# Kernel tuning notes

Measured on AMD Instinct MI355X. Metric: run time of the kernel, lower is better.

Reference implementation:

```python
import jax, jax.numpy as jnp
import numpy as np

B, N, D_IN = 128, 128, 1024
H1, D_OUT = 256, 32
K = 8  # num_clusters


def setup_inputs() -> dict:
    key = jax.random.key(0)
    ks = jax.random.split(key, 3)
    x = jax.random.normal(ks[0], (B, N, D_IN), dtype=jnp.float32)
    W1 = jax.random.normal(ks[1], (D_IN, H1), dtype=jnp.float32) * (1.0 / np.sqrt(D_IN))
    b1 = jnp.zeros((H1,), jnp.float32)
    W2 = jax.random.normal(ks[2], (H1, D_OUT), dtype=jnp.float32) * (1.0 / np.sqrt(H1))
    b2 = jnp.zeros((D_OUT,), jnp.float32)
    return {"x": x, "W1": W1, "b1": b1, "W2": W2, "b2": b2}


def _mlp(x, W1, b1, W2, b2):
    # nn.Sequential(GELU, Linear(1024,256), GELU, Linear(256,32)); torch GELU default = exact erf
    h = jax.nn.gelu(x, approximate=False)
    h = h @ W1 + b1
    h = jax.nn.gelu(h, approximate=False)
    return h @ W2 + b2  # [B, N, 32]


def _ward_labels(feats, k):
    """Greedy ward-linkage agglomerative clustering of feats [n, d] -> int labels [n].
    Ward merge cost d(A,B) = |A||B|/(|A|+|B|) * ||c_A - c_B||^2 (Lance-Williams equiv)."""
    n = feats.shape[0]
    eye = jnp.eye(n, dtype=bool)

    def body(t, state):
        cents, sizes, lab = state
        sq = jnp.sum(cents * cents, axis=-1)
        d2 = jnp.maximum(sq[:, None] + sq[None, :] - 2.0 * (cents @ cents.T), 0.0)
        w = (sizes[:, None] * sizes[None, :]) / (sizes[:, None] + sizes[None, :] + 1e-30)
        active = sizes > 0
        valid = (active[:, None] & active[None, :]) & (~eye)
        Dm = jnp.where(valid, w * d2, jnp.inf)
        idx = jnp.argmin(Dm)
        i, j = idx // n, idx % n
        i2 = jnp.minimum(i, j)
        j2 = jnp.maximum(i, j)
        si, sj = sizes[i2], sizes[j2]
        newc = (cents[i2] * si + cents[j2] * sj) / (si + sj)
        cents = cents.at[i2].set(newc)
        sizes = sizes.at[i2].set(si + sj).at[j2].set(0.0)
        lab = jnp.where(lab == j2, i2, lab)
        return cents, sizes, lab

    init = (feats, jnp.ones((n,), feats.dtype), jnp.arange(n))
    cents, sizes, lab = jax.lax.fori_loop(0, n - k, body, init)
    # relabel surviving representative indices to 0..k-1 (ordered by index)
    rank = jnp.cumsum((sizes > 0).astype(jnp.int32)) - 1
    return rank[lab]


def reference(x, W1, b1, W2, b2):
    feats = _mlp(x, W1, b1, W2, b2)          # [B, N, 32]
    labels = jax.vmap(lambda f: _ward_labels(f, K))(feats)  # [B, N] int32
    return labels
```

## Files before the change

### kernel.cpp

```cpp
#include <hip/hip_runtime.h>
#include <math.h>

#define BB 128
#define NN 128
#define DIN 1024
#define H1 256
#define DOUT 32
#define KCL 8
#define NPTS 128
#define MROWS (BB*NN)
#define CSTR 130
#define RSTR 132
#define HSTR 257
#define DEADKEY 0xFFFFFFFF00000000ull

__device__ __forceinline__ float gelu_exact(float v) {
    return 0.5f * v * (1.0f + erff(v * 0.70710678118654752f));
}

__device__ __forceinline__ unsigned long long mkkey(float v, int r, int j) {
    return ((unsigned long long)__float_as_uint(v) << 32) | (unsigned)((r << 7) | j);
}

__device__ __forceinline__ float readlanef(float v, int lane) {
    return __int_as_float(__builtin_amdgcn_readlane(__float_as_int(v), lane));
}

template<int CTRL, int RMASK>
__device__ __forceinline__ unsigned dpp_umin_step(unsigned v) {
    unsigned t = (unsigned)__builtin_amdgcn_update_dpp((int)v, (int)v, CTRL, RMASK, 0xf, false);
    return t < v ? t : v;
}
__device__ __forceinline__ unsigned wave_umin_bcast(unsigned v) {
    v = dpp_umin_step<0x111, 0xf>(v);
    v = dpp_umin_step<0x112, 0xf>(v);
    v = dpp_umin_step<0x114, 0xf>(v);
    v = dpp_umin_step<0x118, 0xf>(v);
    v = dpp_umin_step<0x142, 0xa>(v);
    v = dpp_umin_step<0x143, 0xc>(v);
    return (unsigned)__builtin_amdgcn_readlane((int)v, 63);
}
__device__ __forceinline__ unsigned half_umin(unsigned v) {
    v = dpp_umin_step<0x111, 0xf>(v);
    v = dpp_umin_step<0x112, 0xf>(v);
    v = dpp_umin_step<0x114, 0xf>(v);
    v = dpp_umin_step<0x118, 0xf>(v);
    v = dpp_umin_step<0x142, 0xa>(v);
    return v;
}

__global__ __launch_bounds__(256) void gelu_kernel(const float* __restrict__ x,
                                                   float* __restrict__ gx, int n4) {
    int i = blockIdx.x * 256 + threadIdx.x;
    const int stride = gridDim.x * 256;
    for (; i < n4; i += stride) {
        float4 v = ((const float4*)x)[i];
        v.x = gelu_exact(v.x);
        v.y = gelu_exact(v.y);
        v.z = gelu_exact(v.z);
        v.w = gelu_exact(v.w);
        ((float4*)gx)[i] = v;
    }
}

template<bool FUSE>
__global__ __launch_bounds__(256) void mlp1_kernel(const float* __restrict__ xin,
                                                   const float* __restrict__ W1,
                                                   const float* __restrict__ b1,
                                                   float* __restrict__ h) {
    __shared__ float As[64][68];
    __shared__ float Bs[64][64];
    const int bn = blockIdx.x;
    const int bm = blockIdx.y;
    const int tid = threadIdx.x;
    const int tx = tid & 15, ty = tid >> 4;

    float acc[4][4] = {{0.f}};

    const int arow = tid >> 2;
    const int kc   = (tid & 3) * 4;
    const int wv   = tid >> 6;
    const int ln   = tid & 63;
    const int bkr  = ln >> 4;
    const int bkc  = (ln & 15) * 4;

    const float* xrow = xin + (size_t)(bm * 64 + arow) * DIN;
    const float* wbase = W1 + bn * 64;

    for (int kt = 0; kt < DIN; kt += 64) {
        float4 a0 = *(const float4*)(xrow + kt + kc);
        float4 a1 = *(const float4*)(xrow + kt + kc + 16);
        float4 a2 = *(const float4*)(xrow + kt + kc + 32);
        float4 a3 = *(const float4*)(xrow + kt + kc + 48);
        __syncthreads();
#pragma unroll
        for (int s = 0; s < 4; ++s) {
            const int kr = wv * 16 + s * 4;
            const float* g = wbase + (size_t)(kt + kr + bkr) * H1 + bkc;
            __builtin_amdgcn_global_load_lds(
                (const __attribute__((address_space(1))) unsigned int*)g,
                (__attribute__((address_space(3))) unsigned int*)&Bs[kr][0], 16, 0, 0);
        }
        if (FUSE) {
            As[kc + 0][arow] = gelu_exact(a0.x);
            As[kc + 1][arow] = gelu_exact(a0.y);
            As[kc + 2][arow] = gelu_exact(a0.z);
            As[kc + 3][arow] = gelu_exact(a0.w);
            As[16 + kc + 0][arow] = gelu_exact(a1.x);
            As[16 + kc + 1][arow] = gelu_exact(a1.y);
            As[16 + kc + 2][arow] = gelu_exact(a1.z);
            As[16 + kc + 3][arow] = gelu_exact(a1.w);
            As[32 + kc + 0][arow] = gelu_exact(a2.x);
            As[32 + kc + 1][arow] = gelu_exact(a2.y);
            As[32 + kc + 2][arow] = gelu_exact(a2.z);
            As[32 + kc + 3][arow] = gelu_exact(a2.w);
            As[48 + kc + 0][arow] = gelu_exact(a3.x);
            As[48 + kc + 1][arow] = gelu_exact(a3.y);
            As[48 + kc + 2][arow] = gelu_exact(a3.z);
            As[48 + kc + 3][arow] = gelu_exact(a3.w);
        } else {
            As[kc + 0][arow] = a0.x;
            As[kc + 1][arow] = a0.y;
            As[kc + 2][arow] = a0.z;
            As[kc + 3][arow] = a0.w;
            As[16 + kc + 0][arow] = a1.x;
            As[16 + kc + 1][arow] = a1.y;
            As[16 + kc + 2][arow] = a1.z;
            As[16 + kc + 3][arow] = a1.w;
            As[32 + kc + 0][arow] = a2.x;
            As[32 + kc + 1][arow] = a2.y;
            As[32 + kc + 2][arow] = a2.z;
            As[32 + kc + 3][arow] = a2.w;
            As[48 + kc + 0][arow] = a3.x;
            As[48 + kc + 1][arow] = a3.y;
            As[48 + kc + 2][arow] = a3.z;
            As[48 + kc + 3][arow] = a3.w;
        }
        __syncthreads();
#pragma unroll
        for (int kk = 0; kk < 64; ++kk) {
            float4 a = *(const float4*)&As[kk][ty * 4];
            float4 b = *(const float4*)&Bs[kk][tx * 4];
            float ar[4] = {a.x, a.y, a.z, a.w};
            float br[4] = {b.x, b.y, b.z, b.w};
#pragma unroll
            for (int i = 0; i < 4; ++i)
#pragma unroll
                for (int j = 0; j < 4; ++j)
                    acc[i][j] = fmaf(ar[i], br[j], acc[i][j]);
        }
    }

    const int row = bm * 64 + ty * 4;
    const int col = bn * 64 + tx * 4;
    float4 bias = *(const float4*)(b1 + col);
#pragma unroll
    for (int i = 0; i < 4; ++i) {
        float4 o;
        o.x = acc[i][0] + bias.x;
        o.y = acc[i][1] + bias.y;
        o.z = acc[i][2] + bias.z;
        o.w = acc[i][3] + bias.w;
        *(float4*)(h + (size_t)(row + i) * H1 + col) = o;
    }
}

__global__ __launch_bounds__(256) void mlp2_kernel(const float* __restrict__ h,
                                                   const float* __restrict__ W2,
                                                   const float* __restrict__ b2,
                                                   float* __restrict__ feats) {
    __shared__ float hs[32 * HSTR];
    __shared__ float w2s[H1 * DOUT];
    const int blk = blockIdx.x;
    const int tid = threadIdx.x;

    for (int i = tid; i < (H1 * DOUT) / 4; i += 256)
        ((float4*)w2s)[i] = ((const float4*)W2)[i];

    const float* hb = h + (size_t)blk * 32 * H1;
    const int sr = tid & 31;
    const int sk = (tid >> 5) * 32;
    const float* hrow = hb + (size_t)sr * H1 + sk;
#pragma unroll
    for (int j = 0; j < 8; ++j) {
        float4 v = ((const float4*)hrow)[j];
        hs[sr * HSTR + sk + 4 * j + 0] = gelu_exact(v.x);
        hs[sr * HSTR + sk + 4 * j + 1] = gelu_exact(v.y);
        hs[sr * HSTR + sk + 4 * j + 2] = gelu_exact(v.z);
        hs[sr * HSTR + sk + 4 * j + 3] = gelu_exact(v.w);
    }
    __syncthreads();

    const int row = tid >> 3;
    const int col4 = (tid & 7) * 4;
    const float4 bias = ((const float4*)b2)[tid & 7];
    float a0 = 0.f, a1 = 0.f, a2 = 0.f, a3 = 0.f;
    const float* hr = &hs[row * HSTR];
    for (int k = 0; k < H1; ++k) {
        float a = hr[k];
        float4 w = *(const float4*)&w2s[k * DOUT + col4];
        a0 = fmaf(a, w.x, a0);
        a1 = fmaf(a, w.y, a1);
        a2 = fmaf(a, w.z, a2);
        a3 = fmaf(a, w.w, a3);
    }
    float4 o;
    o.x = a0 + bias.x;
    o.y = a1 + bias.y;
    o.z = a2 + bias.z;
    o.w = a3 + bias.w;
    *(float4*)(feats + (size_t)(blk * 32 + row) * DOUT + col4) = o;
}

__global__ __launch_bounds__(256) void ward_kernel(const float* __restrict__ feats,
                                                   int* __restrict__ out) {
    __shared__ __align__(16) float cost[NPTS * RSTR];
    __shared__ float centsT[32 * CSTR];
    __shared__ unsigned long long rowkey[NPTS];
    __shared__ float sqArr[NPTS];
    __shared__ float szsE[NPTS];
    __shared__ int rnk[NPTS];

    const int b = blockIdx.x;
    const int tid = threadIdx.x;
    const float* f = feats + (size_t)b * NPTS * DOUT;
    const float INF = __builtin_inff();

    for (int i = tid; i < NPTS * DOUT; i += 256) {
        int r = i >> 5, d = i & 31;
        centsT[d * CSTR + r] = f[i];
    }
    __syncthreads();
    if (tid < NPTS) {
        float s = 0.f;
#pragma unroll
        for (int d = 0; d < 32; ++d) {
            float v = centsT[d * CSTR + tid];
            s = fmaf(v, v, s);
        }
        sqArr[tid] = s;
    }
    __syncthreads();
    {
        int ti = tid >> 4, tj = tid & 15;
        int I0 = ti * 8, J0 = tj * 8;
        float acc[8][8];
#pragma unroll
        for (int u = 0; u < 8; ++u)
#pragma unroll
            for (int v = 0; v < 8; ++v) acc[u][v] = 0.f;
        for (int d = 0; d < 32; ++d) {
            float a[8], bb[8];
#pragma unroll
            for (int u = 0; u < 8; ++u) a[u] = centsT[d * CSTR + I0 + u];
#pragma unroll
            for (int v = 0; v < 8; ++v) bb[v] = centsT[d * CSTR + J0 + v];
#pragma unroll
            for (int u = 0; u < 8; ++u)
#pragma unroll
                for (int v = 0; v < 8; ++v)
                    acc[u][v] = fmaf(a[u], bb[v], acc[u][v]);
        }
#pragma unroll
        for (int u = 0; u < 8; ++u) {
#pragma unroll
            for (int v = 0; v < 8; ++v) {
                int i = I0 + u, j = J0 + v;
                float d2 = sqArr[i] + sqArr[j] - 2.0f * acc[u][v];
                if (d2 < 0.f) d2 = 0.f;
                float w = (1.0f * 1.0f) / (1.0f + 1.0f + 1e-30f);
                cost[i * RSTR + j] = (i == j) ? INF : w * d2;
            }
        }
    }
    __syncthreads();
    if (tid < NPTS) {
        unsigned long long best = DEADKEY;
        for (int j = 0; j < NPTS; ++j) {
            float v = cost[tid * RSTR + j];
            unsigned long long k = mkkey(v, tid, j);
            if (k < best) best = k;
        }
        rowkey[tid] = best;
    }
    __syncthreads();

    if (tid >= 64) return;
    const int lane = tid;
    const int hh = lane & 31;
    const int r0 = lane * 2, r1 = lane * 2 + 1;

    unsigned long long k0 = rowkey[r0], k1 = rowkey[r1];
    float s0 = 1.0f, s1 = 1.0f;
    int lab0 = r0, lab1 = r1;
    unsigned long long alive0 = ~0ull, alive1 = ~0ull;

    for (int it = 0; it < NPTS - KCL; ++it) {
        unsigned bv0 = (unsigned)(k0 >> 32), bv1 = (unsigned)(k1 >> 32);
        unsigned lmin = bv0 < bv1 ? bv0 : bv1;
        unsigned lflat = (bv0 <= bv1) ? (unsigned)(k0 & 0x3FFFu) : (unsigned)(k1 & 0x3FFFu);
        unsigned gmin = wave_umin_bcast(lmin);
        unsigned long long bmask = __ballot(lmin == gmin);
        int lsel = __ffsll(bmask) - 1;
        unsigned flat = (unsigned)__builtin_amdgcn_readlane((int)lflat, lsel);
        int ra = (int)(flat >> 7), ca = (int)(flat & 127u);
        const int i2 = ra < ca ? ra : ca;
        const int j2 = ra < ca ? ca : ra;
        const float Dij = __uint_as_float(gmin);

        float2 ci = *(const float2*)&cost[i2 * RSTR + r0];
        float2 cj = *(const float2*)&cost[j2 * RSTR + r0];

        float si = readlanef((i2 & 1) ? s1 : s0, i2 >> 1);
        float sj = readlanef((j2 & 1) ? s1 : s0, j2 >> 1);
        const float snew = si + sj;

        int arg0 = (int)(k0 & 127u), arg1 = (int)(k1 & 127u);
        bool d0 = (s0 > 0.f) && r0 != i2 && r0 != j2 && (arg0 == i2 || arg0 == j2);
        bool d1 = (s1 > 0.f) && r1 != i2 && r1 != j2 && (arg1 == i2 || arg1 == j2);
        unsigned long long m0 = __ballot(d0), m1 = __ballot(d1);

        float Dn0 = ((si + s0) * ci.x + (sj + s0) * cj.x - s0 * Dij) / (snew + s0);
        float Dn1 = ((si + s1) * ci.y + (sj + s1) * cj.y - s1 * Dij) / (snew + s1);
        if (Dn0 < 0.f) Dn0 = 0.f;
        if (Dn1 < 0.f) Dn1 = 0.f;

        if (lab0 == j2) lab0 = i2;
        if (lab1 == j2) lab1 = i2;
        if (r0 == i2) s0 = snew; else if (r0 == j2) { s0 = 0.f; k0 = DEADKEY; }
        if (r1 == i2) s1 = snew; else if (r1 == j2) { s1 = 0.f; k1 = DEADKEY; }
        if (j2 < 64) alive0 &= ~(1ull << j2); else alive1 &= ~(1ull << (j2 - 64));

        bool w0 = (s0 > 0.f) && r0 != i2 && r0 != j2;
        bool w1 = (s1 > 0.f) && r1 != i2 && r1 != j2;
        if (w0) {
            cost[r0 * RSTR + i2] = Dn0;
            cost[i2 * RSTR + r0] = Dn0;
            if (!d0) {
                unsigned long long nk = mkkey(Dn0, r0, i2);
                if (nk < k0) k0 = nk;
            }
        }
        if (w1) {
            cost[r1 * RSTR + i2] = Dn1;
            cost[i2 * RSTR + r1] = Dn1;
            if (!d1) {
                unsigned long long nk = mkkey(Dn1, r1, i2);
                if (nk < k1) k1 = nk;
            }
        }

        bool pi = true;
        unsigned long long mm0 = m0, mm1 = m1;
        while (pi | (mm0 != 0ull) | (mm1 != 0ull)) {
            int rA, rB;
            bool hasB = false;
            if (pi) { rA = i2; pi = false; }
            else if (mm0) { int t = __ffsll(mm0) - 1; rA = 2 * t; mm0 &= mm0 - 1; }
            else { int t = __ffsll(mm1) - 1; rA = 2 * t + 1; mm1 &= mm1 - 1; }
            if (mm0) { int t = __ffsll(mm0) - 1; rB = 2 * t; mm0 &= mm0 - 1; hasB = true; }
            else if (mm1) { int t = __ffsll(mm1) - 1; rB = 2 * t + 1; mm1 &= mm1 - 1; hasB = true; }
            else rB = rA;

            int r = (lane < 32) ? rA : rB;
            float4 cv = *(const float4*)&cost[r * RSTR + 4 * hh];
            unsigned long long word = (hh < 16) ? alive0 : alive1;
            unsigned nib = (unsigned)(word >> ((4 * hh) & 63)) & 0xFu;
            unsigned e0 = (nib & 1u) ? __float_as_uint(cv.x) : 0xFFFFFFFFu;
            unsigned e1 = (nib & 2u) ? __float_as_uint(cv.y) : 0xFFFFFFFFu;
            unsigned e2 = (nib & 4u) ? __float_as_uint(cv.z) : 0xFFFFFFFFu;
            unsigned e3 = (nib & 8u) ? __float_as_uint(cv.w) : 0xFFFFFFFFu;
            unsigned m = e0; int c = 0;
            if (e1 < m) { m = e1; c = 1; }
            if (e2 < m) { m = e2; c = 2; }
            if (e3 < m) { m = e3; c = 3; }
            int lcol = 4 * hh + c;
            unsigned hm = half_umin(m);
            unsigned vA = (unsigned)__builtin_amdgcn_readlane((int)hm, 31);
            unsigned vB = (unsigned)__builtin_amdgcn_readlane((int)hm, 63);
            unsigned vref = (lane < 32) ? vA : vB;
            unsigned long long msk = __ballot(m == vref);
            int laneA = __ffsll(msk & 0xFFFFFFFFull) - 1;
            int laneB = 32 + __ffsll(msk >> 32) - 1;
            int colA = __builtin_amdgcn_readlane(lcol, laneA);
            int colB = __builtin_amdgcn_readlane(lcol, laneB);
            unsigned long long keyA = ((unsigned long long)vA << 32) | (unsigned)((rA << 7) | colA);
            unsigned long long keyB = ((unsigned long long)vB << 32) | (unsigned)((rB << 7) | colB);
            if (lane == (rA >> 1)) { if (rA & 1) k1 = keyA; else k0 = keyA; }
            if (hasB && lane == (rB >> 1)) { if (rB & 1) k1 = keyB; else k0 = keyB; }
        }
    }

    szsE[r0] = s0;
    szsE[r1] = s1;
    __asm__ volatile("s_waitcnt lgkmcnt(0)" ::: "memory");
    if (lane == 0) {
        int c = 0;
        for (int i = 0; i < NPTS; ++i) rnk[i] = (szsE[i] > 0.f) ? c++ : -1;
    }
    __asm__ volatile("s_waitcnt lgkmcnt(0)" ::: "memory");
    out[b * NPTS + r0] = rnk[lab0];
    out[b * NPTS + r1] = rnk[lab1];
}

extern "C" void kernel_launch(void* const* d_in, const int* in_sizes, int n_in,
                              void* d_out, int out_size, void* d_ws, size_t ws_size,
                              hipStream_t stream) {
    const float* x  = (const float*)d_in[0];
    const float* W1 = (const float*)d_in[1];
    const float* b1 = (const float*)d_in[2];
    const float* W2 = (const float*)d_in[3];
    const float* b2 = (const float*)d_in[4];

    float* h = (float*)d_ws;
    float* feats = h + (size_t)MROWS * H1;
    float* gx = feats + (size_t)MROWS * DOUT;
    int* out = (int*)d_out;

    const size_t need = ((size_t)MROWS * H1 + (size_t)MROWS * DOUT + (size_t)MROWS * DIN) * 4;
    const bool use_gx = ws_size >= need;

    if (use_gx) {
        gelu_kernel<<<2048, 256, 0, stream>>>(x, gx, MROWS * DIN / 4);
        mlp1_kernel<false><<<dim3(H1 / 64, MROWS / 64), 256, 0, stream>>>(gx, W1, b1, h);
    } else {
        mlp1_kernel<true><<<dim3(H1 / 64, MROWS / 64), 256, 0, stream>>>(x, W1, b1, h);
    }
    mlp2_kernel<<<MROWS / 32, 256, 0, stream>>>(h, W2, b2, feats);
    ward_kernel<<<BB, 256, 0, stream>>>(feats, out);
}
```

Baseline: 431.9 us.

## Use split-fp16 MFMA emulation of fp32 GEMM for first MLP layer

```diff
diff --git a/kernel.cpp b/kernel.cpp
--- a/kernel.cpp
+++ b/kernel.cpp
@@ -14,6 +14,10 @@
 #define HSTR 257
 #define DEADKEY 0xFFFFFFFF00000000ull
 
+typedef _Float16 f16;
+typedef f16 f16x8 __attribute__((ext_vector_type(8)));
+typedef float f32x4 __attribute__((ext_vector_type(4)));
+
 __device__ __forceinline__ float gelu_exact(float v) {
     return 0.5f * v * (1.0f + erff(v * 0.70710678118654752f));
 }
@@ -49,21 +53,133 @@
     return v;
 }
 
-__global__ __launch_bounds__(256) void gelu_kernel(const float* __restrict__ x,
-                                                   float* __restrict__ gx, int n4) {
+__device__ __forceinline__ void split3(float g, unsigned short &uh, unsigned short &ul,
+                                       unsigned short &uq) {
+    f16 h = (f16)g;
+    float r = g - (float)h;
+    f16 l = (f16)r;
+    float r2 = r - (float)l;
+    f16 q = (f16)r2;
+    uh = __builtin_bit_cast(unsigned short, h);
+    ul = __builtin_bit_cast(unsigned short, l);
+    uq = __builtin_bit_cast(unsigned short, q);
+}
+
+__global__ __launch_bounds__(256) void prep_kernel(const float* __restrict__ x,
+                                                   unsigned short* __restrict__ gh,
+                                                   unsigned short* __restrict__ gl,
+                                                   unsigned short* __restrict__ gq, int n4) {
     int i = blockIdx.x * 256 + threadIdx.x;
     const int stride = gridDim.x * 256;
     for (; i < n4; i += stride) {
         float4 v = ((const float4*)x)[i];
-        v.x = gelu_exact(v.x);
-        v.y = gelu_exact(v.y);
-        v.z = gelu_exact(v.z);
-        v.w = gelu_exact(v.w);
-        ((float4*)gx)[i] = v;
-    }
-}
-
-template<bool FUSE>
+        ushort4 oh, ol, oq;
+        split3(gelu_exact(v.x), oh.x, ol.x, oq.x);
+        split3(gelu_exact(v.y), oh.y, ol.y, oq.y);
+        split3(gelu_exact(v.z), oh.z, ol.z, oq.z);
+        split3(gelu_exact(v.w), oh.w, ol.w, oq.w);
+        ((ushort4*)gh)[i] = oh;
+        ((ushort4*)gl)[i] = ol;
+        ((ushort4*)gq)[i] = oq;
+    }
+}
+
+__global__ __launch_bounds__(256) void w1prep_kernel(const float* __restrict__ W1,
+                                                     unsigned short* __restrict__ th,
+                                                     unsigned short* __restrict__ tl,
+                                                     unsigned short* __restrict__ tq) {
+    const int n = blockIdx.x * 4 + (threadIdx.x >> 6);
+    const int t = threadIdx.x & 63;
+    unsigned short ah[16], al[16], aq[16];
+#pragma unroll
+    for (int i = 0; i < 16; ++i) {
+        int k = t * 16 + i;
+        split3(W1[(size_t)k * H1 + n], ah[i], al[i], aq[i]);
+    }
+    const size_t base = (size_t)n * DIN + t * 16;
+#pragma unroll
+    for (int j = 0; j < 4; ++j) {
+        *(ushort4*)(th + base + 4 * j) = make_ushort4(ah[4*j], ah[4*j+1], ah[4*j+2], ah[4*j+3]);
+        *(ushort4*)(tl + base + 4 * j) = make_ushort4(al[4*j], al[4*j+1], al[4*j+2], al[4*j+3]);
+        *(ushort4*)(tq + base + 4 * j) = make_ushort4(aq[4*j], aq[4*j+1], aq[4*j+2], aq[4*j+3]);
+    }
+}
+
+__global__ __launch_bounds__(256) void mlp1_mfma(const f16* __restrict__ gxh,
+                                                 const f16* __restrict__ gxl,
+                                                 const f16* __restrict__ gxq,
+                                                 const f16* __restrict__ wth,
+                                                 const f16* __restrict__ wtl,
+                                                 const f16* __restrict__ wtq,
+                                                 const float* __restrict__ b1,
+                                                 float* __restrict__ h) {
+    __shared__ __align__(16) f16 T[6][64 * 32];
+    const int bn = blockIdx.x;
+    const int bm = blockIdx.y;
+    const int tid = threadIdx.x;
+    const int w = tid >> 6, l = tid & 63;
+
+    const f16* pA0 = gxh + (size_t)(bm * 64) * DIN;
+    const f16* pA1 = gxl + (size_t)(bm * 64) * DIN;
+    const f16* pA2 = gxq + (size_t)(bm * 64) * DIN;
+    const f16* pB0 = wth + (size_t)(bn * 64) * DIN;
+    const f16* pB1 = wtl + (size_t)(bn * 64) * DIN;
+    const f16* pB2 = wtq + (size_t)(bn * 64) * DIN;
+
+    f32x4 acc[4];
+#pragma unroll
+    for (int ct = 0; ct < 4; ++ct) acc[ct] = (f32x4){0.f, 0.f, 0.f, 0.f};
+
+    const int grow = l >> 2;
+    const int gcol = (l & 3) * 8;
+    const int fr = l & 15, fk = (l >> 4) * 8;
+
+    for (int kt = 0; kt < DIN; kt += 32) {
+        __syncthreads();
+#define STAGE(T6, SRC)                                                               \
+        {                                                                            \
+            const f16* s = SRC + (size_t)(w * 16 + grow) * DIN + kt + gcol;          \
+            __builtin_amdgcn_global_load_lds(                                        \
+                (const __attribute__((address_space(1))) unsigned int*)s,            \
+                (__attribute__((address_space(3))) unsigned int*)&T[T6][w * 512],    \
+                16, 0, 0);                                                           \
+        }
+        STAGE(0, pA0) STAGE(1, pA1) STAGE(2, pA2)
+        STAGE(3, pB0) STAGE(4, pB1) STAGE(5, pB2)
+#undef STAGE
+        __syncthreads();
+
+        f16x8 Ah = *(const f16x8*)&T[0][(w * 16 + fr) * 32 + fk];
+        f16x8 Al = *(const f16x8*)&T[1][(w * 16 + fr) * 32 + fk];
+        f16x8 Aq = *(const f16x8*)&T[2][(w * 16 + fr) * 32 + fk];
+#pragma unroll
+        for (int ct = 0; ct < 4; ++ct) {
+            f16x8 Bh = *(const f16x8*)&T[3][(ct * 16 + fr) * 32 + fk];
+            f16x8 Bl = *(const f16x8*)&T[4][(ct * 16 + fr) * 32 + fk];
+            f16x8 Bq = *(const f16x8*)&T[5][(ct * 16 + fr) * 32 + fk];
+            f32x4 a = acc[ct];
+            a = __builtin_amdgcn_mfma_f32_16x16x32_f16(Ah, Bh, a, 0, 0, 0);
+            a = __builtin_amdgcn_mfma_f32_16x16x32_f16(Ah, Bl, a, 0, 0, 0);
+            a = __builtin_amdgcn_mfma_f32_16x16x32_f16(Al, Bh, a, 0, 0, 0);
+            a = __builtin_amdgcn_mfma_f32_16x16x32_f16(Ah, Bq, a, 0, 0, 0);
+            a = __builtin_amdgcn_mfma_f32_16x16x32_f16(Aq, Bh, a, 0, 0, 0);
+            a = __builtin_amdgcn_mfma_f32_16x16x32_f16(Al, Bl, a, 0, 0, 0);
+            acc[ct] = a;
+        }
+    }
+
+    const int orow = bm * 64 + w * 16 + (l >> 4) * 4;
+    const int ocol0 = bn * 64 + (l & 15);
+#pragma unroll
+    for (int ct = 0; ct < 4; ++ct) {
+        const int col = ocol0 + ct * 16;
+        const float bias = b1[col];
+#pragma unroll
+        for (int r = 0; r < 4; ++r)
+            h[(size_t)(orow + r) * H1 + col] = acc[ct][r] + bias;
+    }
+}
+
 __global__ __launch_bounds__(256) void mlp1_kernel(const float* __restrict__ xin,
                                                    const float* __restrict__ W1,
                                                    const float* __restrict__ b1,
@@ -76,13 +192,12 @@
     const int tx = tid & 15, ty = tid >> 4;
 
     float acc[4][4] = {{0.f}};
-
     const int arow = tid >> 2;
-    const int kc   = (tid & 3) * 4;
-    const int wv   = tid >> 6;
-    const int ln   = tid & 63;
-    const int bkr  = ln >> 4;
-    const int bkc  = (ln & 15) * 4;
+    const int kc = (tid & 3) * 4;
+    const int wv = tid >> 6;
+    const int ln = tid & 63;
+    const int bkr = ln >> 4;
+    const int bkc = (ln & 15) * 4;
 
     const float* xrow = xin + (size_t)(bm * 64 + arow) * DIN;
     const float* wbase = W1 + bn * 64;
@@ -101,41 +216,22 @@
                 (const __attribute__((address_space(1))) unsigned int*)g,
                 (__attribute__((address_space(3))) unsigned int*)&Bs[kr][0], 16, 0, 0);
         }
-        if (FUSE) {
-            As[kc + 0][arow] = gelu_exact(a0.x);
-            As[kc + 1][arow] = gelu_exact(a0.y);
-            As[kc + 2][arow] = gelu_exact(a0.z);
-            As[kc + 3][arow] = gelu_exact(a0.w);
-            As[16 + kc + 0][arow] = gelu_exact(a1.x);
-            As[16 + kc + 1][arow] = gelu_exact(a1.y);
-            As[16 + kc + 2][arow] = gelu_exact(a1.z);
-            As[16 + kc + 3][arow] = gelu_exact(a1.w);
-            As[32 + kc + 0][arow] = gelu_exact(a2.x);
-            As[32 + kc + 1][arow] = gelu_exact(a2.y);
-            As[32 + kc + 2][arow] = gelu_exact(a2.z);
-            As[32 + kc + 3][arow] = gelu_exact(a2.w);
-            As[48 + kc + 0][arow] = gelu_exact(a3.x);
-            As[48 + kc + 1][arow] = gelu_exact(a3.y);
-            As[48 + kc + 2][arow] = gelu_exact(a3.z);
-            As[48 + kc + 3][arow] = gelu_exact(a3.w);
-        } else {
-            As[kc + 0][arow] = a0.x;
-            As[kc + 1][arow] = a0.y;
-            As[kc + 2][arow] = a0.z;
-            As[kc + 3][arow] = a0.w;
-            As[16 + kc + 0][arow] = a1.x;
-            As[16 + kc + 1][arow] = a1.y;
-            As[16 + kc + 2][arow] = a1.z;
-            As[16 + kc + 3][arow] = a1.w;
-            As[32 + kc + 0][arow] = a2.x;
-            As[32 + kc + 1][arow] = a2.y;
-            As[32 + kc + 2][arow] = a2.z;
-            As[32 + kc + 3][arow] = a2.w;
-            As[48 + kc + 0][arow] = a3.x;
-            As[48 + kc + 1][arow] = a3.y;
-            As[48 + kc + 2][arow] = a3.z;
-            As[48 + kc + 3][arow] = a3.w;
-        }
+        As[kc + 0][arow] = gelu_exact(a0.x);
+        As[kc + 1][arow] = gelu_exact(a0.y);
+        As[kc + 2][arow] = gelu_exact(a0.z);
+        As[kc + 3][arow] = gelu_exact(a0.w);
+        As[16 + kc + 0][arow] = gelu_exact(a1.x);
+        As[16 + kc + 1][arow] = gelu_exact(a1.y);
+        As[16 + kc + 2][arow] = gelu_exact(a1.z);
+        As[16 + kc + 3][arow] = gelu_exact(a1.w);
+        As[32 + kc + 0][arow] = gelu_exact(a2.x);
+        As[32 + kc + 1][arow] = gelu_exact(a2.y);
+        As[32 + kc + 2][arow] = gelu_exact(a2.z);
+        As[32 + kc + 3][arow] = gelu_exact(a2.w);
+        As[48 + kc + 0][arow] = gelu_exact(a3.x);
+        As[48 + kc + 1][arow] = gelu_exact(a3.y);
+        As[48 + kc + 2][arow] = gelu_exact(a3.z);
+        As[48 + kc + 3][arow] = gelu_exact(a3.w);
         __syncthreads();
 #pragma unroll
         for (int kk = 0; kk < 64; ++kk) {
@@ -411,20 +507,28 @@
     const float* b1 = (const float*)d_in[2];
     const float* W2 = (const float*)d_in[3];
     const float* b2 = (const float*)d_in[4];
+    int* out = (int*)d_out;
 
     float* h = (float*)d_ws;
     float* feats = h + (size_t)MROWS * H1;
-    float* gx = feats + (size_t)MROWS * DOUT;
-    int* out = (int*)d_out;
-
-    const size_t need = ((size_t)MROWS * H1 + (size_t)MROWS * DOUT + (size_t)MROWS * DIN) * 4;
-    const bool use_gx = ws_size >= need;
-
-    if (use_gx) {
-        gelu_kernel<<<2048, 256, 0, stream>>>(x, gx, MROWS * DIN / 4);
-        mlp1_kernel<false><<<dim3(H1 / 64, MROWS / 64), 256, 0, stream>>>(gx, W1, b1, h);
+    unsigned short* gxh = (unsigned short*)(feats + (size_t)MROWS * DOUT);
+    unsigned short* gxl = gxh + (size_t)MROWS * DIN;
+    unsigned short* gxq = gxl + (size_t)MROWS * DIN;
+    unsigned short* wth = gxq + (size_t)MROWS * DIN;
+    unsigned short* wtl = wth + (size_t)H1 * DIN;
+    unsigned short* wtq = wtl + (size_t)H1 * DIN;
+
+    const size_t need_mfma = ((size_t)MROWS * H1 + (size_t)MROWS * DOUT) * 4 +
+                             (size_t)MROWS * DIN * 2 * 3 + (size_t)H1 * DIN * 2 * 3;
+
+    if (ws_size >= need_mfma) {
+        prep_kernel<<<2048, 256, 0, stream>>>(x, gxh, gxl, gxq, MROWS * DIN / 4);
+        w1prep_kernel<<<64, 256, 0, stream>>>(W1, wth, wtl, wtq);
+        mlp1_mfma<<<dim3(4, 256), 256, 0, stream>>>(
+            (const f16*)gxh, (const f16*)gxl, (const f16*)gxq,
+            (const f16*)wth, (const f16*)wtl, (const f16*)wtq, b1, h);
     } else {
-        mlp1_kernel<true><<<dim3(H1 / 64, MROWS / 64), 256, 0, stream>>>(x, W1, b1, h);
+        mlp1_kernel<<<dim3(4, 256), 256, 0, stream>>>(x, W1, b1, h);
     }
     mlp2_kernel<<<MROWS / 32, 256, 0, stream>>>(h, W2, b2, feats);
     ward_kernel<<<BB, 256, 0, stream>>>(feats, out);
```

Measured after the change: 387.2 us. -10.3%, faster.
